# Optimization experiments

Measured on AMD Instinct MI355X. Metric: run time of the kernel, lower is better.

The kernel has to match this reference:

```python
import jax, jax.numpy as jnp
import numpy as np

TEMP = 50.0  # softmax temperature from __init__ (temp=50.0)

N_SAMPLES = 32768
NUM_CANDIDATES = 2048
NUM_DIMS = 16


def setup_inputs() -> dict:
    key = jax.random.key(0)
    k1, k2, k3 = jax.random.split(key, 3)
    X = jax.random.normal(k1, (N_SAMPLES, NUM_DIMS), dtype=jnp.float32)
    Y = jax.random.normal(k2, (1, NUM_CANDIDATES, NUM_DIMS), dtype=jnp.float32)  # Y_rest param
    b = jax.random.normal(k3, (1, NUM_CANDIDATES), dtype=jnp.float32) * 0.1     # intercept_rest param
    return {"X": X, "Y": Y, "b": b}


def reference(X, Y, b):
    """FiniteModel.forward in convex mode with soft selection.

    scores[n, c] = <X[n], Y[0, c]> - b[0, c]           (dot-product kernel)
    weights      = softmax(temp * scores, axis=1)       (moded_max, soft mode)
    f_x[n]       = sum_c weights[n, c] * scores[n, c]
    choice[n, :] = sum_c weights[n, c] * Y[0, c, :]
    Returns (choice, f_x) as in the torch forward.
    """
    Yc = Y[0]                                     # [C, D]
    scores = jnp.einsum('nd,cd->nc', X, Yc) - b   # [N, C] (b broadcasts from [1, C])
    weights = jax.nn.softmax(TEMP * scores, axis=1)
    f_x = jnp.sum(weights * scores, axis=1)       # [N]
    choice = jnp.einsum('nc,cd->nd', weights, Yc) # [N, D]
    return choice, f_x
```

## Files before the change

kernel.cpp:

```cpp
#include <hip/hip_runtime.h>
#include <math.h>

#if defined(__has_builtin)
#  if __has_builtin(__builtin_amdgcn_exp2f)
#    define EXP2F(x) __builtin_amdgcn_exp2f(x)
#  else
#    define EXP2F(x) exp2f(x)
#  endif
#else
#  define EXP2F(x) exp2f(x)
#endif

constexpr int   DD = 16;
constexpr float T2 = 72.13475204444817f;
constexpr float DEFER_THR = 8.0f;

typedef __attribute__((ext_vector_type(8)))  short s16x8;
typedef __attribute__((ext_vector_type(16))) float f32x16;

static __device__ __forceinline__ s16x8 mk8(unsigned a, unsigned b, unsigned c, unsigned d) {
    union { unsigned u[4]; s16x8 v; } x;
    x.u[0] = a; x.u[1] = b; x.u[2] = c; x.u[3] = d;
    return x.v;
}
static __device__ __forceinline__ unsigned pack_tr(float a, float b) {
    return (__float_as_uint(a) >> 16) | (__float_as_uint(b) & 0xFFFF0000u);
}
static __device__ __forceinline__ float trunc_bf(float a) {
    return __uint_as_float(__float_as_uint(a) & 0xFFFF0000u);
}
static __device__ __forceinline__ unsigned short rne16(float f) {
    unsigned u = __float_as_uint(f);
    return (unsigned short)((u + 0x7FFFu + ((u >> 16) & 1u)) >> 16);
}
static __device__ __forceinline__ float bfh2f(unsigned short h) {
    return __uint_as_float(((unsigned)h) << 16);
}

__global__ void prep_kernel(const float* __restrict__ Y, const float* __restrict__ B,
                            unsigned short* __restrict__ YhA, unsigned short* __restrict__ YlA,
                            unsigned short* __restrict__ VhP, unsigned short* __restrict__ VlP,
                            float* __restrict__ bRp, unsigned* __restrict__ Bq, int C)
{
    int c = blockIdx.x * blockDim.x + threadIdx.x;
    if (c >= C) return;

    int c15 = c & 15;
    int j    = (c15 & 3) | (((c15 >> 3) & 1) << 2);
    int hslt = (c15 >> 2) & 1;
    int slot = (c & ~15) | (hslt << 3) | j;

    const float* yr = Y + (size_t)c * DD;
#pragma unroll
    for (int d = 0; d < DD; ++d) {
        float y = yr[d];
        unsigned short h = rne16(y);
        unsigned short l = rne16(y - bfh2f(h));
        YhA[(size_t)c * DD + d] = h;
        YlA[(size_t)c * DD + d] = l;
        VhP[(size_t)d * C + slot] = h;
        VlP[(size_t)d * C + slot] = l;
    }
#pragma unroll
    for (int r = DD; r < 32; ++r) {
        VhP[(size_t)r * C + slot] = 0;
        VlP[(size_t)r * C + slot] = 0;
    }

    float bb = B[c];
    int t = c >> 5, w5 = c & 31;
    int rr = (w5 & 3) | ((w5 >> 3) << 2);
    int hh = (w5 >> 2) & 1;
    bRp[t * 32 + hh * 16 + rr] = bb;

    float qb = -T2 * bb;
    unsigned short qh = rne16(qb);
    unsigned short ql = rne16(qb - bfh2f(qh));
    Bq[c] = (unsigned)qh | ((unsigned)ql << 16);
}

__global__ __launch_bounds__(256, 4)
void finite_mfma(const float* __restrict__ X,
                 const unsigned short* __restrict__ YhA, const unsigned short* __restrict__ YlA,
                 const unsigned short* __restrict__ VhP, const unsigned short* __restrict__ VlP,
                 const float* __restrict__ bRp, const unsigned* __restrict__ Bq,
                 float* __restrict__ out, int N, int C)
{
    const int tid  = threadIdx.x;
    const int wave = tid >> 6, lane = tid & 63;
    const int s = lane & 31, hi = lane >> 5;
    const int n0 = blockIdx.x * 32;
    const int cpw = C >> 2, cbase = wave * cpw, ntile = cpw >> 5;

    __shared__ float bufc[4][16][32];
    __shared__ float lds_l[4][32], lds_fx[4][32], lds_m[4][32];

    const float* xp = X + ((size_t)(n0 + s) * DD + 8 * hi);
    float xq[8];
#pragma unroll
    for (int jj = 0; jj < 8; ++jj) xq[jj] = xp[jj] * T2;
    unsigned xhw[4], xlw[4];
#pragma unroll
    for (int jj = 0; jj < 4; ++jj) {
        float a = xq[2 * jj], b = xq[2 * jj + 1];
        xhw[jj] = pack_tr(a, b);
        xlw[jj] = pack_tr(a - trunc_bf(a), b - trunc_bf(b));
    }
    const s16x8 xqh = mk8(xhw[0], xhw[1], xhw[2], xhw[3]);
    const s16x8 xql = mk8(xlw[0], xlw[1], xlw[2], xlw[3]);
    const s16x8 ones2 = mk8(hi ? 0u : 0x3F803F80u, 0u, 0u, 0u);

    f32x16 acc;
#pragma unroll
    for (int r = 0; r < 16; ++r) acc[r] = 0.0f;
    float m2 = -INFINITY, lacc = 0.0f, fxb = 0.0f;

    const size_t vrow = (size_t)s * C;

    for (int t = 0; t < ntile; ++t) {
        const int c0 = cbase + t * 32;
        const s16x8 aYh = *(const s16x8*)(YhA + (size_t)(c0 + s) * DD + 8 * hi);
        const s16x8 aYl = *(const s16x8*)(YlA + (size_t)(c0 + s) * DD + 8 * hi);
        const unsigned bw = Bq[c0 + s];
        const s16x8 a2 = mk8(hi ? 0u : bw, 0u, 0u, 0u);
        const s16x8 vh0 = *(const s16x8*)(VhP + vrow + c0 + 8 * hi);
        const s16x8 vh1 = *(const s16x8*)(VhP + vrow + c0 + 16 + 8 * hi);
        const s16x8 vl0 = *(const s16x8*)(VlP + vrow + c0 + 8 * hi);
        const s16x8 vl1 = *(const s16x8*)(VlP + vrow + c0 + 16 + 8 * hi);
        const float4* brp = (const float4*)(bRp + (size_t)(c0 >> 5) * 32 + hi * 16);
        const float4 br0 = brp[0], br1 = brp[1], br2 = brp[2], br3 = brp[3];

        f32x16 S;
#pragma unroll
        for (int r = 0; r < 16; ++r) S[r] = 0.0f;
        S = __builtin_amdgcn_mfma_f32_32x32x16_bf16(a2,  ones2, S, 0, 0, 0);
        S = __builtin_amdgcn_mfma_f32_32x32x16_bf16(aYh, xqh,   S, 0, 0, 0);
        S = __builtin_amdgcn_mfma_f32_32x32x16_bf16(aYh, xql,   S, 0, 0, 0);
        S = __builtin_amdgcn_mfma_f32_32x32x16_bf16(aYl, xqh,   S, 0, 0, 0);

        float tmax = S[0];
#pragma unroll
        for (int r = 1; r < 16; ++r) tmax = fmaxf(tmax, S[r]);
        tmax = fmaxf(tmax, __shfl_xor(tmax, 32, 64));

        if (__any(tmax > m2 + DEFER_THR)) {
            float nm = fmaxf(m2, tmax);
            float sc = EXP2F(m2 - nm);
#pragma unroll
            for (int r = 0; r < 16; ++r) acc[r] *= sc;
            lacc *= sc; fxb *= sc;
            m2 = nm;
        }

        float e[16];
#pragma unroll
        for (int r = 0; r < 16; ++r) e[r] = EXP2F(S[r] - m2);

        const float bR[16] = {br0.x, br0.y, br0.z, br0.w, br1.x, br1.y, br1.z, br1.w,
                              br2.x, br2.y, br2.z, br2.w, br3.x, br3.y, br3.z, br3.w};
#pragma unroll
        for (int r = 0; r < 16; ++r) {
            lacc += e[r];
            fxb = fmaf(e[r], bR[r], fxb);
        }

        unsigned phw[8], plw[8];
#pragma unroll
        for (int jj = 0; jj < 8; ++jj) {
            float a = e[2 * jj], b = e[2 * jj + 1];
            phw[jj] = pack_tr(a, b);
            plw[jj] = pack_tr(a - trunc_bf(a), b - trunc_bf(b));
        }
        const s16x8 Bph0 = mk8(phw[0], phw[1], phw[2], phw[3]);
        const s16x8 Bpl0 = mk8(plw[0], plw[1], plw[2], plw[3]);
        const s16x8 Bph1 = mk8(phw[4], phw[5], phw[6], phw[7]);
        const s16x8 Bpl1 = mk8(plw[4], plw[5], plw[6], plw[7]);

        acc = __builtin_amdgcn_mfma_f32_32x32x16_bf16(vh0, Bph0, acc, 0, 0, 0);
        acc = __builtin_amdgcn_mfma_f32_32x32x16_bf16(vl0, Bph0, acc, 0, 0, 0);
        acc = __builtin_amdgcn_mfma_f32_32x32x16_bf16(vh0, Bpl0, acc, 0, 0, 0);
        acc = __builtin_amdgcn_mfma_f32_32x32x16_bf16(vh1, Bph1, acc, 0, 0, 0);
        acc = __builtin_amdgcn_mfma_f32_32x32x16_bf16(vl1, Bph1, acc, 0, 0, 0);
        acc = __builtin_amdgcn_mfma_f32_32x32x16_bf16(vh1, Bpl1, acc, 0, 0, 0);
    }

    float l2 = lacc + __shfl_xor(lacc, 32, 64);
    float f2 = fxb  + __shfl_xor(fxb,  32, 64);

    if (hi == 0) lds_m[wave][s] = m2;
    __syncthreads();
    float mstar = fmaxf(fmaxf(lds_m[0][s], lds_m[1][s]), fmaxf(lds_m[2][s], lds_m[3][s]));
    float sw = EXP2F(m2 - mstar);
#pragma unroll
    for (int r = 0; r < 8; ++r) {
        int dv = (r & 3) + 8 * (r >> 2) + 4 * hi;
        bufc[wave][dv][s] = acc[r] * sw;
    }
    if (hi == 0) { lds_l[wave][s] = l2 * sw; lds_fx[wave][s] = f2 * sw; }
    __syncthreads();

#pragma unroll
    for (int q = 0; q < 2; ++q) {
        int u = tid + 256 * q;
        int dv = u >> 5, ss = u & 31;
        bufc[0][dv][ss] = bufc[0][dv][ss] + bufc[1][dv][ss] + bufc[2][dv][ss] + bufc[3][dv][ss];
    }
    if (tid < 32) {
        lds_l[0][tid]  = lds_l[0][tid]  + lds_l[1][tid]  + lds_l[2][tid]  + lds_l[3][tid];
        lds_fx[0][tid] = lds_fx[0][tid] + lds_fx[1][tid] + lds_fx[2][tid] + lds_fx[3][tid];
    }
    __syncthreads();

    {
        int ss = tid >> 3, d0 = (tid & 7) * 2;
        float inv = 1.0f / lds_l[0][ss];
        float2 o = make_float2(bufc[0][d0][ss] * inv, bufc[0][d0 + 1][ss] * inv);
        *(float2*)(out + (size_t)(n0 + ss) * DD + d0) = o;
    }
    if (tid < 32) {
        float inv = 1.0f / lds_l[0][tid];
        const float* xr = X + (size_t)(n0 + tid) * DD;
        float dot = 0.0f;
#pragma unroll
        for (int d = 0; d < DD; ++d) dot = fmaf(xr[d], bufc[0][d][tid], dot);
        out[(size_t)N * DD + n0 + tid] = (dot - lds_fx[0][tid]) * inv;
    }
}

extern "C" void kernel_launch(void* const* d_in, const int* in_sizes, int n_in,
                              void* d_out, int out_size, void* d_ws, size_t ws_size,
                              hipStream_t stream) {
    const float* X = (const float*)d_in[0];
    const float* Y = (const float*)d_in[1];
    const float* B = (const float*)d_in[2];
    float*     out = (float*)d_out;

    const int N = in_sizes[0] / DD;
    const int C = in_sizes[2];

    char* w = (char*)d_ws;
    unsigned short* YhA = (unsigned short*)(w);
    unsigned short* YlA = (unsigned short*)(w + (size_t)C * DD * 2);
    unsigned short* VhP = (unsigned short*)(w + (size_t)C * DD * 4);
    unsigned short* VlP = (unsigned short*)(w + (size_t)C * DD * 4 + (size_t)32 * C * 2);
    float*          bRp = (float*)      (w + (size_t)C * DD * 4 + (size_t)32 * C * 4);
    unsigned*       Bq  = (unsigned*)   (w + (size_t)C * DD * 4 + (size_t)32 * C * 4 + (size_t)C * 4);

    hipLaunchKernelGGL(prep_kernel, dim3((C + 255) / 256), dim3(256), 0, stream,
                       Y, B, YhA, YlA, VhP, VlP, bRp, Bq, C);
    hipLaunchKernelGGL(finite_mfma, dim3(N / 32), dim3(256), 0, stream,
                       X, YhA, YlA, VhP, VlP, bRp, Bq, out, N, C);
}
```

Baseline: 102.6 us.

## Fold softmax sum and bias dot into MFMA padding rows; double-buffer fragment loads

The bias and a constant-one row are packed into the previously zero padding rows 16 and 17 of the V operand. The existing P·V MFMAs then yield the softmax denominator and the bias-weighted sum directly. This removes the per-tile scalar exp sums, the bias FMAs and the bRp float4 loads, along with their LDS reduction arrays. The tile loop is also software-pipelined with two fragment register sets, so loads for the next tile are issued before the current one is processed. In exchange, the denominator and bias sums are now accumulated through bf16 hi/lo splits, and the extra live fragment set raises register pressure.

```diff
diff --git a/kernel.cpp b/kernel.cpp
--- a/kernel.cpp
+++ b/kernel.cpp
@@ -40,7 +40,7 @@
 __global__ void prep_kernel(const float* __restrict__ Y, const float* __restrict__ B,
                             unsigned short* __restrict__ YhA, unsigned short* __restrict__ YlA,
                             unsigned short* __restrict__ VhP, unsigned short* __restrict__ VlP,
-                            float* __restrict__ bRp, unsigned* __restrict__ Bq, int C)
+                            unsigned* __restrict__ Bq, int C)
 {
     int c = blockIdx.x * blockDim.x + threadIdx.x;
     if (c >= C) return;
@@ -61,17 +61,17 @@
         VhP[(size_t)d * C + slot] = h;
         VlP[(size_t)d * C + slot] = l;
     }
-#pragma unroll
-    for (int r = DD; r < 32; ++r) {
+    float bb = B[c];
+    unsigned short bh = rne16(bb);
+    VhP[(size_t)16 * C + slot] = bh;
+    VlP[(size_t)16 * C + slot] = rne16(bb - bfh2f(bh));
+    VhP[(size_t)17 * C + slot] = 0x3F80;
+    VlP[(size_t)17 * C + slot] = 0;
+#pragma unroll
+    for (int r = 18; r < 32; ++r) {
         VhP[(size_t)r * C + slot] = 0;
         VlP[(size_t)r * C + slot] = 0;
     }
-
-    float bb = B[c];
-    int t = c >> 5, w5 = c & 31;
-    int rr = (w5 & 3) | ((w5 >> 3) << 2);
-    int hh = (w5 >> 2) & 1;
-    bRp[t * 32 + hh * 16 + rr] = bb;
 
     float qb = -T2 * bb;
     unsigned short qh = rne16(qb);
@@ -79,11 +79,16 @@
     Bq[c] = (unsigned)qh | ((unsigned)ql << 16);
 }
 
+struct Frag {
+    s16x8 aYh, aYl, vh0, vh1, vl0, vl1;
+    unsigned bw;
+};
+
 __global__ __launch_bounds__(256, 4)
 void finite_mfma(const float* __restrict__ X,
                  const unsigned short* __restrict__ YhA, const unsigned short* __restrict__ YlA,
                  const unsigned short* __restrict__ VhP, const unsigned short* __restrict__ VlP,
-                 const float* __restrict__ bRp, const unsigned* __restrict__ Bq,
+                 const unsigned* __restrict__ Bq,
                  float* __restrict__ out, int N, int C)
 {
     const int tid  = threadIdx.x;
@@ -92,8 +97,14 @@
     const int n0 = blockIdx.x * 32;
     const int cpw = C >> 2, cbase = wave * cpw, ntile = cpw >> 5;
 
-    __shared__ float bufc[4][16][32];
-    __shared__ float lds_l[4][32], lds_fx[4][32], lds_m[4][32];
+    __shared__ float bufc[4][18][32];
+    __shared__ float lds_m[4][32];
+
+    const unsigned short* pYh = YhA + ((size_t)(cbase + s) * DD + 8 * hi);
+    const unsigned short* pYl = YlA + ((size_t)(cbase + s) * DD + 8 * hi);
+    const unsigned short* pVh = VhP + ((size_t)s * C + cbase + 8 * hi);
+    const unsigned short* pVl = VlP + ((size_t)s * C + cbase + 8 * hi);
+    const unsigned*       pBq = Bq + cbase + s;
 
     const float* xp = X + ((size_t)(n0 + s) * DD + 8 * hi);
     float xq[8];
@@ -113,79 +124,68 @@
     f32x16 acc;
 #pragma unroll
     for (int r = 0; r < 16; ++r) acc[r] = 0.0f;
-    float m2 = -INFINITY, lacc = 0.0f, fxb = 0.0f;
-
-    const size_t vrow = (size_t)s * C;
-
-    for (int t = 0; t < ntile; ++t) {
-        const int c0 = cbase + t * 32;
-        const s16x8 aYh = *(const s16x8*)(YhA + (size_t)(c0 + s) * DD + 8 * hi);
-        const s16x8 aYl = *(const s16x8*)(YlA + (size_t)(c0 + s) * DD + 8 * hi);
-        const unsigned bw = Bq[c0 + s];
-        const s16x8 a2 = mk8(hi ? 0u : bw, 0u, 0u, 0u);
-        const s16x8 vh0 = *(const s16x8*)(VhP + vrow + c0 + 8 * hi);
-        const s16x8 vh1 = *(const s16x8*)(VhP + vrow + c0 + 16 + 8 * hi);
-        const s16x8 vl0 = *(const s16x8*)(VlP + vrow + c0 + 8 * hi);
-        const s16x8 vl1 = *(const s16x8*)(VlP + vrow + c0 + 16 + 8 * hi);
-        const float4* brp = (const float4*)(bRp + (size_t)(c0 >> 5) * 32 + hi * 16);
-        const float4 br0 = brp[0], br1 = brp[1], br2 = brp[2], br3 = brp[3];
-
-        f32x16 S;
-#pragma unroll
-        for (int r = 0; r < 16; ++r) S[r] = 0.0f;
-        S = __builtin_amdgcn_mfma_f32_32x32x16_bf16(a2,  ones2, S, 0, 0, 0);
-        S = __builtin_amdgcn_mfma_f32_32x32x16_bf16(aYh, xqh,   S, 0, 0, 0);
-        S = __builtin_amdgcn_mfma_f32_32x32x16_bf16(aYh, xql,   S, 0, 0, 0);
-        S = __builtin_amdgcn_mfma_f32_32x32x16_bf16(aYl, xqh,   S, 0, 0, 0);
-
-        float tmax = S[0];
-#pragma unroll
-        for (int r = 1; r < 16; ++r) tmax = fmaxf(tmax, S[r]);
-        tmax = fmaxf(tmax, __shfl_xor(tmax, 32, 64));
-
-        if (__any(tmax > m2 + DEFER_THR)) {
-            float nm = fmaxf(m2, tmax);
-            float sc = EXP2F(m2 - nm);
-#pragma unroll
-            for (int r = 0; r < 16; ++r) acc[r] *= sc;
-            lacc *= sc; fxb *= sc;
-            m2 = nm;
-        }
-
-        float e[16];
-#pragma unroll
-        for (int r = 0; r < 16; ++r) e[r] = EXP2F(S[r] - m2);
-
-        const float bR[16] = {br0.x, br0.y, br0.z, br0.w, br1.x, br1.y, br1.z, br1.w,
-                              br2.x, br2.y, br2.z, br2.w, br3.x, br3.y, br3.z, br3.w};
-#pragma unroll
-        for (int r = 0; r < 16; ++r) {
-            lacc += e[r];
-            fxb = fmaf(e[r], bR[r], fxb);
-        }
-
-        unsigned phw[8], plw[8];
-#pragma unroll
-        for (int jj = 0; jj < 8; ++jj) {
-            float a = e[2 * jj], b = e[2 * jj + 1];
-            phw[jj] = pack_tr(a, b);
-            plw[jj] = pack_tr(a - trunc_bf(a), b - trunc_bf(b));
-        }
-        const s16x8 Bph0 = mk8(phw[0], phw[1], phw[2], phw[3]);
-        const s16x8 Bpl0 = mk8(plw[0], plw[1], plw[2], plw[3]);
-        const s16x8 Bph1 = mk8(phw[4], phw[5], phw[6], phw[7]);
-        const s16x8 Bpl1 = mk8(plw[4], plw[5], plw[6], plw[7]);
-
-        acc = __builtin_amdgcn_mfma_f32_32x32x16_bf16(vh0, Bph0, acc, 0, 0, 0);
-        acc = __builtin_amdgcn_mfma_f32_32x32x16_bf16(vl0, Bph0, acc, 0, 0, 0);
-        acc = __builtin_amdgcn_mfma_f32_32x32x16_bf16(vh0, Bpl0, acc, 0, 0, 0);
-        acc = __builtin_amdgcn_mfma_f32_32x32x16_bf16(vh1, Bph1, acc, 0, 0, 0);
-        acc = __builtin_amdgcn_mfma_f32_32x32x16_bf16(vl1, Bph1, acc, 0, 0, 0);
-        acc = __builtin_amdgcn_mfma_f32_32x32x16_bf16(vh1, Bpl1, acc, 0, 0, 0);
-    }
-
-    float l2 = lacc + __shfl_xor(lacc, 32, 64);
-    float f2 = fxb  + __shfl_xor(fxb,  32, 64);
+    float m2 = -INFINITY;
+
+#define LDF(F, k) do {                                              \
+        (F).aYh = *(const s16x8*)(pYh + (size_t)(k) * 512);         \
+        (F).aYl = *(const s16x8*)(pYl + (size_t)(k) * 512);         \
+        (F).vh0 = *(const s16x8*)(pVh + (size_t)(k) * 32);          \
+        (F).vh1 = *(const s16x8*)(pVh + (size_t)(k) * 32 + 16);     \
+        (F).vl0 = *(const s16x8*)(pVl + (size_t)(k) * 32);          \
+        (F).vl1 = *(const s16x8*)(pVl + (size_t)(k) * 32 + 16);     \
+        (F).bw  = pBq[(size_t)(k) * 32];                            \
+    } while (0)
+
+#define PROC(F) do {                                                            \
+        const s16x8 a2 = mk8(hi ? 0u : (F).bw, 0u, 0u, 0u);                     \
+        f32x16 S;                                                               \
+        _Pragma("unroll")                                                       \
+        for (int r = 0; r < 16; ++r) S[r] = 0.0f;                               \
+        S = __builtin_amdgcn_mfma_f32_32x32x16_bf16(a2,     ones2, S, 0, 0, 0); \
+        S = __builtin_amdgcn_mfma_f32_32x32x16_bf16((F).aYh, xqh,  S, 0, 0, 0); \
+        S = __builtin_amdgcn_mfma_f32_32x32x16_bf16((F).aYh, xql,  S, 0, 0, 0); \
+        S = __builtin_amdgcn_mfma_f32_32x32x16_bf16((F).aYl, xqh,  S, 0, 0, 0); \
+        float tmax = S[0];                                                      \
+        _Pragma("unroll")                                                       \
+        for (int r = 1; r < 16; ++r) tmax = fmaxf(tmax, S[r]);                  \
+        tmax = fmaxf(tmax, __shfl_xor(tmax, 32, 64));                           \
+        if (__any(tmax > m2 + DEFER_THR)) {                                     \
+            float nm = fmaxf(m2, tmax);                                         \
+            float sc = EXP2F(m2 - nm);                                          \
+            _Pragma("unroll")                                                   \
+            for (int r = 0; r < 16; ++r) acc[r] *= sc;                          \
+            m2 = nm;                                                            \
+        }                                                                       \
+        unsigned phw[8], plw[8];                                                \
+        _Pragma("unroll")                                                       \
+        for (int jj = 0; jj < 8; ++jj) {                                        \
+            float e0 = EXP2F(S[2 * jj] - m2);                                   \
+            float e1 = EXP2F(S[2 * jj + 1] - m2);                               \
+            phw[jj] = pack_tr(e0, e1);                                          \
+            plw[jj] = pack_tr(e0 - trunc_bf(e0), e1 - trunc_bf(e1));            \
+        }                                                                       \
+        const s16x8 Bph0 = mk8(phw[0], phw[1], phw[2], phw[3]);                 \
+        const s16x8 Bpl0 = mk8(plw[0], plw[1], plw[2], plw[3]);                 \
+        const s16x8 Bph1 = mk8(phw[4], phw[5], phw[6], phw[7]);                 \
+        const s16x8 Bpl1 = mk8(plw[4], plw[5], plw[6], plw[7]);                 \
+        acc = __builtin_amdgcn_mfma_f32_32x32x16_bf16((F).vh0, Bph0, acc, 0, 0, 0); \
+        acc = __builtin_amdgcn_mfma_f32_32x32x16_bf16((F).vl0, Bph0, acc, 0, 0, 0); \
+        acc = __builtin_amdgcn_mfma_f32_32x32x16_bf16((F).vh0, Bpl0, acc, 0, 0, 0); \
+        acc = __builtin_amdgcn_mfma_f32_32x32x16_bf16((F).vh1, Bph1, acc, 0, 0, 0); \
+        acc = __builtin_amdgcn_mfma_f32_32x32x16_bf16((F).vl1, Bph1, acc, 0, 0, 0); \
+        acc = __builtin_amdgcn_mfma_f32_32x32x16_bf16((F).vh1, Bpl1, acc, 0, 0, 0); \
+    } while (0)
+
+    Frag f0, f1;
+    LDF(f0, 0);
+    for (int t = 0; t < ntile; t += 2) {
+        LDF(f1, t + 1);
+        PROC(f0);
+        if (t + 2 < ntile) LDF(f0, t + 2);
+        PROC(f1);
+    }
+#undef LDF
+#undef PROC
 
     if (hi == 0) lds_m[wave][s] = m2;
     __syncthreads();
@@ -196,34 +196,36 @@
         int dv = (r & 3) + 8 * (r >> 2) + 4 * hi;
         bufc[wave][dv][s] = acc[r] * sw;
     }
-    if (hi == 0) { lds_l[wave][s] = l2 * sw; lds_fx[wave][s] = f2 * sw; }
+    if (hi == 0) {
+        bufc[wave][16][s] = acc[8] * sw;
+        bufc[wave][17][s] = acc[9] * sw;
+    }
     __syncthreads();
 
 #pragma unroll
-    for (int q = 0; q < 2; ++q) {
+    for (int q = 0; q < 3; ++q) {
         int u = tid + 256 * q;
-        int dv = u >> 5, ss = u & 31;
-        bufc[0][dv][ss] = bufc[0][dv][ss] + bufc[1][dv][ss] + bufc[2][dv][ss] + bufc[3][dv][ss];
-    }
-    if (tid < 32) {
-        lds_l[0][tid]  = lds_l[0][tid]  + lds_l[1][tid]  + lds_l[2][tid]  + lds_l[3][tid];
-        lds_fx[0][tid] = lds_fx[0][tid] + lds_fx[1][tid] + lds_fx[2][tid] + lds_fx[3][tid];
+        if (u < 18 * 32) {
+            int dv = u >> 5, ss = u & 31;
+            bufc[0][dv][ss] = bufc[0][dv][ss] + bufc[1][dv][ss]
+                            + bufc[2][dv][ss] + bufc[3][dv][ss];
+        }
     }
     __syncthreads();
 
     {
         int ss = tid >> 3, d0 = (tid & 7) * 2;
-        float inv = 1.0f / lds_l[0][ss];
+        float inv = 1.0f / bufc[0][17][ss];
         float2 o = make_float2(bufc[0][d0][ss] * inv, bufc[0][d0 + 1][ss] * inv);
         *(float2*)(out + (size_t)(n0 + ss) * DD + d0) = o;
     }
     if (tid < 32) {
-        float inv = 1.0f / lds_l[0][tid];
+        float inv = 1.0f / bufc[0][17][tid];
         const float* xr = X + (size_t)(n0 + tid) * DD;
         float dot = 0.0f;
 #pragma unroll
         for (int d = 0; d < DD; ++d) dot = fmaf(xr[d], bufc[0][d][tid], dot);
-        out[(size_t)N * DD + n0 + tid] = (dot - lds_fx[0][tid]) * inv;
+        out[(size_t)N * DD + n0 + tid] = (dot - bufc[0][16][tid]) * inv;
     }
 }
 
@@ -243,11 +245,10 @@
     unsigned short* YlA = (unsigned short*)(w + (size_t)C * DD * 2);
     unsigned short* VhP = (unsigned short*)(w + (size_t)C * DD * 4);
     unsigned short* VlP = (unsigned short*)(w + (size_t)C * DD * 4 + (size_t)32 * C * 2);
-    float*          bRp = (float*)      (w + (size_t)C * DD * 4 + (size_t)32 * C * 4);
-    unsigned*       Bq  = (unsigned*)   (w + (size_t)C * DD * 4 + (size_t)32 * C * 4 + (size_t)C * 4);
+    unsigned*       Bq  = (unsigned*)   (w + (size_t)C * DD * 4 + (size_t)32 * C * 4);
 
     hipLaunchKernelGGL(prep_kernel, dim3((C + 255) / 256), dim3(256), 0, stream,
-                       Y, B, YhA, YlA, VhP, VlP, bRp, Bq, C);
+                       Y, B, YhA, YlA, VhP, VlP, Bq, C);
     hipLaunchKernelGGL(finite_mfma, dim3(N / 32), dim3(256), 0, stream,
-                       X, YhA, YlA, VhP, VlP, bRp, Bq, out, N, C);
-}
+                       X, YhA, YlA, VhP, VlP, Bq, out, N, C);
+}
```

Measured after the change: 95.73 us. 1.07x faster.
